# Kernel tuning notes

Measured on AMD Instinct MI355X. Metric: run time of the kernel, lower is better.

## Reference

```python
import jax, jax.numpy as jnp
import numpy as np

B, T, E, H2, V, NT = 256, 192, 300, 256, 11626, 13  # batch, max_len, embed, hidden_dim, vocab, num_tags
START, STOP = 0, 10
NEG = -10000.0


def setup_inputs() -> dict:
    key = jax.random.key(0)
    ks = jax.random.split(key, 13)
    H = H2 // 2
    s = 0.1
    trans = jax.random.normal(ks[12], (NT, NT), dtype=jnp.float32)
    trans = trans.at[START, :].set(NEG).at[:, STOP].set(NEG)
    return {
        "sentence": jax.random.randint(ks[0], (B, T), 0, V),
        "seq_len": jax.random.randint(ks[1], (B,), 1, T + 1),  # lengths >= 1
        "tags": jax.random.randint(ks[2], (B, T), 0, 10),
        "embedding": jax.random.normal(ks[3], (V, E), dtype=jnp.float32) * s,
        "W_ih_f": jax.random.normal(ks[4], (4 * H, E), dtype=jnp.float32) * s,
        "W_hh_f": jax.random.normal(ks[5], (4 * H, H), dtype=jnp.float32) * s,
        "b_f": jnp.zeros((4 * H,), jnp.float32),
        "W_ih_b": jax.random.normal(ks[6], (4 * H, E), dtype=jnp.float32) * s,
        "W_hh_b": jax.random.normal(ks[7], (4 * H, H), dtype=jnp.float32) * s,
        "b_b": jnp.zeros((4 * H,), jnp.float32),
        "W_fc": jax.random.normal(ks[8], (NT, H2), dtype=jnp.float32) * s,
        "b_fc": jnp.zeros((NT,), jnp.float32),
        "transitions": trans,
    }


def _rev_within_len(x, lens):
    # reverse each sequence's first `len` positions (mimics packed-sequence reverse dir)
    t = jnp.arange(x.shape[1])
    idx = jnp.where(t[None, :] < lens[:, None], lens[:, None] - 1 - t[None, :], t[None, :])
    return jnp.take_along_axis(x, idx[:, :, None], axis=1)


def _lstm_dir(x, lens, W_ih, W_hh, b):
    # x: [B,T,E] -> [B,T,H]; PyTorch gate order i,f,g,o; padded steps frozen + zeroed output
    Bx, Tx, _ = x.shape
    H = W_hh.shape[1]
    mask = (jnp.arange(Tx)[None, :] < lens[:, None]).astype(x.dtype)  # [B,T]
    gx = jnp.einsum('bte,ge->btg', x, W_ih) + b  # precompute input projections

    def step(carry, inp):
        h, c = carry
        g_x, m = inp  # [B,4H], [B,1]
        g = g_x + h @ W_hh.T
        i, f, gg, o = jnp.split(g, 4, axis=-1)
        c_new = jax.nn.sigmoid(f) * c + jax.nn.sigmoid(i) * jnp.tanh(gg)
        h_new = jax.nn.sigmoid(o) * jnp.tanh(c_new)
        h = jnp.where(m > 0, h_new, h)
        c = jnp.where(m > 0, c_new, c)
        return (h, c), h * m

    h0 = jnp.zeros((Bx, H), x.dtype)
    _, hs = jax.lax.scan(step, (h0, h0), (gx.transpose(1, 0, 2), mask.T[:, :, None]))
    return hs.transpose(1, 0, 2)


def _crf_nll(feats, tags, transitions):
    # feats: [B,T,NT]; iterate over ALL T padded positions (faithful to source)
    def fwd_step(alpha, feat):
        # alpha_new[b,j] = logsumexp_i(alpha[b,i] + trans[j,i]) + feat[b,j]
        nxt = jax.nn.logsumexp(alpha[:, None, :] + transitions[None, :, :], axis=-1) + feat
        return nxt, None

    alpha0 = jnp.full((feats.shape[0], NT), NEG, feats.dtype).at[:, START].set(0.0)
    alphaT, _ = jax.lax.scan(fwd_step, alpha0, feats.transpose(1, 0, 2))
    fwd_score = jax.nn.logsumexp(alphaT + transitions[STOP][None, :], axis=-1)  # [B]

    tags_ext = jnp.concatenate([jnp.full((feats.shape[0], 1), START, tags.dtype), tags], axis=1)
    trans_sc = transitions[tags_ext[:, 1:], tags_ext[:, :-1]].sum(-1)
    emit_sc = jnp.take_along_axis(feats, tags[:, :, None], axis=2)[:, :, 0].sum(-1)
    gold = trans_sc + emit_sc + transitions[STOP, tags[:, -1]]
    return fwd_score - gold  # [B]


def reference(sentence, seq_len, tags, embedding, W_ih_f, W_hh_f, b_f,
              W_ih_b, W_hh_b, b_b, W_fc, b_fc, transitions):
    lens = jnp.clip(seq_len, 1, T)  # seq_len.clamp(max=192)
    emb = embedding[sentence]  # [B,T,E]
    h_f = _lstm_dir(emb, lens, W_ih_f, W_hh_f, b_f)
    h_b = _rev_within_len(_lstm_dir(_rev_within_len(emb, lens), lens, W_ih_b, W_hh_b, b_b), lens)
    out = jnp.concatenate([h_f, h_b], axis=-1)  # [B,T,H2]
    feats = jnp.einsum('bth,gh->btg', out, W_fc) + b_fc  # [B,T,NT]
    nll = _crf_nll(feats, tags, transitions)
    return nll.mean()
```

## Files before the change

kernel.cpp:

```cpp
#include <hip/hip_runtime.h>
#include <hip/hip_bf16.h>


#define B_   256
#define T_   192
#define E_   300
#define KP   320
#define H_   128
#define G4   512
#define NG   1024
#define NT_  13
#define NEGV -10000.0f
#define HSTR 144

typedef __attribute__((ext_vector_type(8))) short bf16x8;
typedef __attribute__((ext_vector_type(4))) float f32x4;
typedef __attribute__((ext_vector_type(4))) unsigned short u16x4;

__device__ __forceinline__ unsigned short f2bf(float f) {
    return (unsigned short)(__float_as_uint(f) >> 16);
}
__device__ __forceinline__ float bf2f(unsigned short h) {
    return __uint_as_float(((unsigned)h) << 16);
}
__device__ __forceinline__ float sigf(float x) {
    return __builtin_amdgcn_rcpf(1.0f + __expf(-x));
}
__device__ __forceinline__ float tanhfast(float x) {
    return __builtin_amdgcn_rcpf(1.0f + __expf(-2.0f * x)) * 2.0f - 1.0f;
}
__device__ __forceinline__ void barrier_lgkm() {
    asm volatile("s_waitcnt lgkmcnt(0)\n\ts_barrier" ::: "memory");
}

__global__ void pack_kernel(const float* __restrict__ Wf, const float* __restrict__ Wb,
                            const float* __restrict__ Whf, const float* __restrict__ Whb,
                            const float* __restrict__ emb, const int* __restrict__ sent,
                            unsigned short* __restrict__ Wp, unsigned short* __restrict__ Whp,
                            unsigned short* __restrict__ A, float* __restrict__ out) {
    int blk = blockIdx.x;
    int k = threadIdx.x;
    if (blk == 0 && k == 0) out[0] = 0.0f;
    if (blk < NG) {
        float v = 0.0f;
        if (k < E_) v = (blk < G4) ? Wf[blk * E_ + k] : Wb[(blk - G4) * E_ + k];
        Wp[blk * KP + k] = f2bf(v);
    } else if (blk < NG + 1024) {
        int t = blk - NG;
        int d = t >> 9, g = t & 511;
        if (k < H_) {
            const float* src = d ? Whb : Whf;
            float v = src[g * H_ + k];
            int w = (g >> 4) & 7, j = g >> 7, colq = g & 15;
            int kc = k >> 5, quad = (k >> 3) & 3, e = k & 7;
            Whp[((((size_t)(d * 8 + w) * 4 + j) * 4 + kc) * 64 + quad * 16 + colq) * 8 + e] = f2bf(v);
        }
    } else {
        int m = blk - NG - 1024;
        int tok = sent[m];
        float v = 0.0f;
        if (k < E_) v = emb[(size_t)tok * E_ + k];
        A[(size_t)m * KP + k] = f2bf(v);
    }
}

__global__ __launch_bounds__(256, 3) void gemm_kernel(const unsigned short* __restrict__ A,
                                                      const unsigned short* __restrict__ Bw,
                                                      const float* __restrict__ bF,
                                                      const float* __restrict__ bB,
                                                      unsigned short* __restrict__ C) {
    __shared__ __align__(16) unsigned short As[128 * 64];
    __shared__ __align__(16) unsigned short Bs[128 * 64];
    const int tid  = threadIdx.x;
    const int lane = tid & 63;
    const int wave = tid >> 6;
    const int wr = wave >> 1, wc = wave & 1;
    const int colL = lane & 15;
    const int mBase = blockIdx.y * 128;
    const int bx = blockIdx.x;
    const int d  = bx >> 2;
    const int w0 = (bx & 3) * 2;
    f32x4 acc[4][4] = {};
    for (int k0 = 0; k0 < KP; k0 += 64) {
        #pragma unroll
        for (int j = 0; j < 4; j++) {
            int c   = tid + 256 * j;
            int row = c >> 3;
            int col = (c & 7) * 8;
            __builtin_amdgcn_global_load_lds(
                (const void*)(A + (size_t)(mBase + row) * KP + k0 + col),
                (void*)((char*)As + c * 16), 16, 0, 0);
            int ws = row >> 6, jj = (row >> 4) & 3, cc = row & 15;
            int srcrow = d * 512 + (8 * jj + w0 + ws) * 16 + cc;
            __builtin_amdgcn_global_load_lds(
                (const void*)(Bw + (size_t)srcrow * KP + k0 + col),
                (void*)((char*)Bs + c * 16), 16, 0, 0);
        }
        __syncthreads();
        #pragma unroll
        for (int ks = 0; ks < 2; ks++) {
            bf16x8 af[4], bfr[4];
            #pragma unroll
            for (int i = 0; i < 4; i++) {
                int arow = wr * 64 + i * 16 + colL;
                af[i]  = *(const bf16x8*)(As + arow * 64 + ks * 32 + (lane >> 4) * 8);
                int brow = wc * 64 + i * 16 + colL;
                bfr[i] = *(const bf16x8*)(Bs + brow * 64 + ks * 32 + (lane >> 4) * 8);
            }
            #pragma unroll
            for (int i = 0; i < 4; i++)
                #pragma unroll
                for (int n2 = 0; n2 < 4; n2++)
                    acc[i][n2] = __builtin_amdgcn_mfma_f32_16x16x32_bf16(af[i], bfr[n2], acc[i][n2], 0, 0, 0);
        }
        __syncthreads();
    }
    const float* bias_d = d ? bB : bF;
    float bj[4];
    #pragma unroll
    for (int n2 = 0; n2 < 4; n2++) bj[n2] = bias_d[(8 * n2 + w0 + wc) * 16 + colL];
    #pragma unroll
    for (int i = 0; i < 4; i++)
        #pragma unroll
        for (int r = 0; r < 4; r++) {
            int row = mBase + wr * 64 + i * 16 + (lane >> 4) * 4 + r;
            u16x4 v;
            #pragma unroll
            for (int n2 = 0; n2 < 4; n2++) v[n2] = f2bf(acc[i][n2][r] + bj[n2]);
            *(u16x4*)(C + (size_t)row * NG + d * 512 + (w0 + wc) * 64 + colL * 4) = v;
        }
}

__global__ __launch_bounds__(576, 1) void lstm_kernel(const unsigned short* __restrict__ gxP,
                                                      const unsigned short* __restrict__ Whp,
                                                      const int* __restrict__ seq_len,
                                                      const float* __restrict__ Wfc,
                                                      float* __restrict__ featsF,
                                                      float* __restrict__ featsB) {
    __shared__ __align__(16) unsigned short hL[2][16 * HSTR];
    __shared__ int Ls[4];
    __shared__ int maxLs;
    const int tid  = threadIdx.x;
    const int wave = tid >> 6;
    const int lane = tid & 63;
    const int col  = lane & 15;
    const int quad = lane >> 4;
    const int dir  = blockIdx.x & 1;
    const int b0   = (blockIdx.x >> 1) * 4;
    float* fOut = dir ? featsB : featsF;

    if (tid < 4) Ls[tid] = min(max(seq_len[b0 + tid], 1), T_);
    __syncthreads();
    if (tid == 0) { int m = 0; for (int i = 0; i < 4; i++) m = max(m, Ls[i]); maxLs = m; }
    __syncthreads();
    const int maxL = maxLs;
    const int Lq = Ls[quad];
    const int dNG = dir ? -NG : NG;

    bf16x8 Bf[4][4];
    bf16x8 Wf8[4];
    const unsigned short* rb = nullptr;
    int ofs2 = 0;
    u16x4 gx0v = {}, gx1v = {};
    float* fb = nullptr;
    int foff = 0;

    if (wave < 8) {
        #pragma unroll
        for (int j = 0; j < 4; j++)
            #pragma unroll
            for (int kc = 0; kc < 4; kc++)
                Bf[j][kc] = *(const bf16x8*)(Whp +
                    ((((size_t)(dir * 8 + wave) * 4 + j) * 4 + kc) * 64 + lane) * 8);
        int row = b0 + quad;
        int p0 = dir ? (Lq - 1) : 0;
        rb = gxP + ((size_t)(row * T_ + p0)) * NG + dir * 512 + wave * 64 + col * 4;
        gx0v = *(const u16x4*)(rb);
        gx1v = *(const u16x4*)(rb + ((Lq > 1) ? dNG : 0));
        ofs2 = min(2, Lq - 1) * dNG;
    } else {
        #pragma unroll
        for (int kc = 0; kc < 4; kc++)
            #pragma unroll
            for (int e = 0; e < 8; e++) {
                float v = (col < NT_) ? Wfc[col * 256 + dir * H_ + kc * 32 + quad * 8 + e] : 0.0f;
                Wf8[kc][e] = (short)f2bf(v);
            }
        fb = fOut + (size_t)(b0 + quad) * T_ * NT_ + col;
        foff = (dir ? (Lq - 1) : 0) * NT_;
    }
    const int fd = dir ? -NT_ : NT_;

    float cst = 0.0f;
    bf16x8 Af[4];
    #pragma unroll
    for (int kc = 0; kc < 4; kc++)
        #pragma unroll
        for (int e = 0; e < 8; e++) Af[kc][e] = 0;

    auto step_body = [&](int s, u16x4& gxs, int par) {
        if (wave < 8) {
            f32x4 acc[4];
            #pragma unroll
            for (int j = 0; j < 4; j++) {
                acc[j][0] = bf2f(gxs[j]);
                acc[j][1] = 0.f; acc[j][2] = 0.f; acc[j][3] = 0.f;
            }
            gxs = *(const u16x4*)(rb + ofs2);
            ofs2 = (s + 3 < Lq) ? ofs2 + dNG : ofs2;
            #pragma unroll
            for (int kc = 0; kc < 4; kc++)
                #pragma unroll
                for (int j = 0; j < 4; j++)
                    acc[j] = __builtin_amdgcn_mfma_f32_16x16x32_bf16(Af[kc], Bf[j][kc], acc[j], 0, 0, 0);
            float cn = sigf(acc[1][0]) * cst + sigf(acc[0][0]) * tanhfast(acc[2][0]);
            cst = cn;
            float hn = sigf(acc[3][0]) * tanhfast(cn);
            hL[par][(quad * 4) * HSTR + wave * 16 + col] = f2bf(hn);
        }
        barrier_lgkm();
        #pragma unroll
        for (int kc = 0; kc < 4; kc++)
            Af[kc] = *(const bf16x8*)(&hL[par][col * HSTR + kc * 32 + quad * 8]);
        if (wave == 8) {
            f32x4 fc = (f32x4){0.f, 0.f, 0.f, 0.f};
            #pragma unroll
            for (int kc = 0; kc < 4; kc++)
                fc = __builtin_amdgcn_mfma_f32_16x16x32_bf16(Af[kc], Wf8[kc], fc, 0, 0, 0);
            if (col < NT_ && s < Lq) fb[foff] = fc[0];
            foff += fd;
        }
    };

    for (int s = 0; s < maxL; s += 2) {
        step_body(s, gx0v, 0);
        if (s + 1 < maxL) step_body(s + 1, gx1v, 1);
    }
}

__global__ __launch_bounds__(64) void crf_kernel(const float* __restrict__ fF,
                                                 const float* __restrict__ fB,
                                                 const float* __restrict__ bfc,
                                                 const float* __restrict__ trans,
                                                 const int* __restrict__ tags,
                                                 const int* __restrict__ seq_len,
                                                 float* __restrict__ out) {
    __shared__ __align__(16) float feat_lds[2 * 208];
    __shared__ float Tlds[NT_ * NT_];
    const int lane = threadIdx.x;
    const int b = blockIdx.x;
    const int Lb = min(max(seq_len[b], 1), T_);
    const float* fFb = fF + (size_t)b * T_ * NT_;
    const float* fBb = fB + (size_t)b * T_ * NT_;
    const int* tg = tags + (size_t)b * T_;

    for (int i = lane; i < NT_ * NT_; i += 64) Tlds[i] = trans[i];

    const int jc = min(lane, NT_ - 1);
    float Tj[NT_];
    #pragma unroll
    for (int i = 0; i < NT_; i++) Tj[i] = trans[jc * NT_ + i];
    const float bj  = bfc[jc];
    const float T10 = trans[10 * NT_ + jc];
    float alj = (jc == 0 && lane == 0) ? 0.0f : NEGV;

    const int e0 = lane * 4;
    const bool ldact = (lane < 52);
    float4 vF = {}, vB = {};
    if (ldact) { vF = *(const float4*)(fFb + e0); vB = *(const float4*)(fBb + e0); }

    #pragma unroll 1
    for (int c = 0; c < 12; ++c) {
        if (ldact) {
            float4 w;
            #pragma unroll
            for (int k = 0; k < 4; k++) {
                unsigned g = (unsigned)(c * 208 + e0 + k);
                unsigned t = g / 13u;
                float s = ((const float*)&vF)[k] + ((const float*)&vB)[k];
                ((float*)&w)[k] = (t < (unsigned)Lb) ? s : 0.0f;
            }
            *(float4*)&feat_lds[(c & 1) * 208 + e0] = w;
            if (c < 11) {
                vF = *(const float4*)(fFb + (c + 1) * 208 + e0);
                vB = *(const float4*)(fBb + (c + 1) * 208 + e0);
            }
        }
        barrier_lgkm();
        const int fbase = (c & 1) * 208;
        for (int tt = 0; tt < 16; ++tt) {
            float a0  = __shfl(alj, 0, 64),  a1  = __shfl(alj, 1, 64);
            float a2  = __shfl(alj, 2, 64),  a3  = __shfl(alj, 3, 64);
            float a4  = __shfl(alj, 4, 64),  a5  = __shfl(alj, 5, 64);
            float a6  = __shfl(alj, 6, 64),  a7  = __shfl(alj, 7, 64);
            float a8  = __shfl(alj, 8, 64),  a9  = __shfl(alj, 9, 64);
            float a10 = __shfl(alj, 10, 64), a11 = __shfl(alj, 11, 64);
            float a12 = __shfl(alj, 12, 64);
            float feat = feat_lds[fbase + tt * NT_ + jc];
            float v0 = a0 + Tj[0],  v1 = a1 + Tj[1],  v2 = a2 + Tj[2],  v3 = a3 + Tj[3];
            float v4 = a4 + Tj[4],  v5 = a5 + Tj[5],  v6 = a6 + Tj[6],  v7 = a7 + Tj[7];
            float v8 = a8 + Tj[8],  v9 = a9 + Tj[9],  v10 = a10 + Tj[10], v11 = a11 + Tj[11];
            float v12 = a12 + Tj[12];
            float p0 = fmaxf(v0, v1), p1 = fmaxf(v2, v3), p2 = fmaxf(v4, v5);
            float p3 = fmaxf(v6, v7), p4 = fmaxf(v8, v9), p5 = fmaxf(v10, v11);
            float q0 = fmaxf(p0, p1), q1 = fmaxf(p2, p3), q2 = fmaxf(p4, p5);
            float m = fmaxf(fmaxf(q0, q1), fmaxf(q2, v12));
            float e0_ = __expf(v0 - m),  e1_ = __expf(v1 - m),  e2_ = __expf(v2 - m);
            float e3_ = __expf(v3 - m),  e4_ = __expf(v4 - m),  e5_ = __expf(v5 - m);
            float e6_ = __expf(v6 - m),  e7_ = __expf(v7 - m),  e8_ = __expf(v8 - m);
            float e9_ = __expf(v9 - m),  e10_ = __expf(v10 - m), e11_ = __expf(v11 - m);
            float e12_ = __expf(v12 - m);
            float s0 = e0_ + e1_, s1 = e2_ + e3_, s2 = e4_ + e5_, s3 = e6_ + e7_;
            float s4 = e8_ + e9_, s5 = e10_ + e11_;
            float u0 = s0 + s1, u1 = s2 + s3, u2 = s4 + s5;
            float ss = (u0 + u1) + (u2 + e12_);
            alj = m + __logf(ss) + feat + bj;
        }
    }

    float gp = 0.0f;
    #pragma unroll
    for (int u = 0; u < 3; ++u) {
        int t = lane + u * 64;
        int tt_ = tg[t];
        int pv = (t == 0) ? 0 : tg[t - 1];
        float e = bfc[tt_];
        if (t < Lb) e += fFb[t * NT_ + tt_] + fBb[t * NT_ + tt_];
        gp += Tlds[tt_ * NT_ + pv] + e;
    }
    #pragma unroll
    for (int o = 32; o > 0; o >>= 1) gp += __shfl_down(gp, o, 64);

    float vj = (lane < NT_) ? (alj + T10) : -3.0e38f;
    float mm = vj;
    #pragma unroll
    for (int o = 32; o > 0; o >>= 1) mm = fmaxf(mm, __shfl_down(mm, o, 64));
    mm = __shfl(mm, 0, 64);
    float se = (lane < NT_) ? __expf(vj - mm) : 0.0f;
    #pragma unroll
    for (int o = 32; o > 0; o >>= 1) se += __shfl_down(se, o, 64);
    if (lane == 0) {
        float fwd = mm + __logf(se);
        float gold = gp + Tlds[10 * NT_ + tg[T_ - 1]];
        atomicAdd(out, (fwd - gold) * (1.0f / 256.0f));
    }
}

extern "C" void kernel_launch(void* const* d_in, const int* in_sizes, int n_in,
                              void* d_out, int out_size, void* d_ws, size_t ws_size,
                              hipStream_t stream) {
    const int*   sentence  = (const int*)d_in[0];
    const int*   seq_len   = (const int*)d_in[1];
    const int*   tags      = (const int*)d_in[2];
    const float* embedding = (const float*)d_in[3];
    const float* W_ih_f    = (const float*)d_in[4];
    const float* W_hh_f    = (const float*)d_in[5];
    const float* b_f       = (const float*)d_in[6];
    const float* W_ih_b    = (const float*)d_in[7];
    const float* W_hh_b    = (const float*)d_in[8];
    const float* b_b       = (const float*)d_in[9];
    const float* W_fc      = (const float*)d_in[10];
    const float* b_fc      = (const float*)d_in[11];
    const float* trans     = (const float*)d_in[12];
    float* out = (float*)d_out;

    char* ws = (char*)d_ws;
    const size_t M = (size_t)B_ * T_;
    unsigned short* Wp    = (unsigned short*)(ws);
    unsigned short* Ap    = (unsigned short*)(ws + 655360);
    unsigned short* gx    = (unsigned short*)(ws + 32112640);
    float* featsF = (float*)(ws + 132775936);
    float* featsB = (float*)(ws + 135331840);
    unsigned short* Whp   = (unsigned short*)(ws + 137887744);

    pack_kernel<<<NG + 1024 + (int)M, KP, 0, stream>>>(W_ih_f, W_ih_b, W_hh_f, W_hh_b,
                                                       embedding, sentence, Wp, Whp, Ap, out);
    dim3 gg(8, (int)(M / 128));
    gemm_kernel<<<gg, 256, 0, stream>>>(Ap, Wp, b_f, b_b, gx);
    lstm_kernel<<<128, 576, 0, stream>>>(gx, Whp, seq_len, W_fc, featsF, featsB);
    crf_kernel<<<B_, 64, 0, stream>>>(featsF, featsB, b_fc, trans, tags, seq_len, out);
}
```

Baseline: 329.6 us.

## Gather embeddings inside GEMM from packed vocab table; process two batches per CRF block

The pack kernel now converts the whole embedding table (V rows) to bf16 instead of materialising a gathered B*T activation matrix. The GEMM gathers rows by token id directly into LDS, which removes a large write and read of the intermediate. The CRF kernel handles two sequences per wavefront, interleaving their independent recurrences to hide shuffle and transcendental latency, at the cost of half as many blocks.

```diff
diff --git a/kernel.cpp b/kernel.cpp
--- a/kernel.cpp
+++ b/kernel.cpp
@@ -6,6 +6,7 @@
 #define T_   192
 #define E_   300
 #define KP   320
+#define V_   11626
 #define H_   128
 #define G4   512
 #define NG   1024
@@ -35,9 +36,9 @@
 
 __global__ void pack_kernel(const float* __restrict__ Wf, const float* __restrict__ Wb,
                             const float* __restrict__ Whf, const float* __restrict__ Whb,
-                            const float* __restrict__ emb, const int* __restrict__ sent,
+                            const float* __restrict__ emb,
                             unsigned short* __restrict__ Wp, unsigned short* __restrict__ Whp,
-                            unsigned short* __restrict__ A, float* __restrict__ out) {
+                            unsigned short* __restrict__ Ep, float* __restrict__ out) {
     int blk = blockIdx.x;
     int k = threadIdx.x;
     if (blk == 0 && k == 0) out[0] = 0.0f;
@@ -56,15 +57,14 @@
             Whp[((((size_t)(d * 8 + w) * 4 + j) * 4 + kc) * 64 + quad * 16 + colq) * 8 + e] = f2bf(v);
         }
     } else {
-        int m = blk - NG - 1024;
-        int tok = sent[m];
-        float v = 0.0f;
-        if (k < E_) v = emb[(size_t)tok * E_ + k];
-        A[(size_t)m * KP + k] = f2bf(v);
-    }
-}
-
-__global__ __launch_bounds__(256, 3) void gemm_kernel(const unsigned short* __restrict__ A,
+        int r = blk - NG - 1024;
+        float v = (k < E_) ? emb[(size_t)r * E_ + k] : 0.0f;
+        Ep[(size_t)r * KP + k] = f2bf(v);
+    }
+}
+
+__global__ __launch_bounds__(256, 3) void gemm_kernel(const unsigned short* __restrict__ Ep,
+                                                      const int* __restrict__ sent,
                                                       const unsigned short* __restrict__ Bw,
                                                       const float* __restrict__ bF,
                                                       const float* __restrict__ bB,
@@ -80,6 +80,10 @@
     const int bx = blockIdx.x;
     const int d  = bx >> 2;
     const int w0 = (bx & 3) * 2;
+    int toks[4];
+    #pragma unroll
+    for (int j = 0; j < 4; j++)
+        toks[j] = sent[mBase + ((tid + 256 * j) >> 3)];
     f32x4 acc[4][4] = {};
     for (int k0 = 0; k0 < KP; k0 += 64) {
         #pragma unroll
@@ -88,7 +92,7 @@
             int row = c >> 3;
             int col = (c & 7) * 8;
             __builtin_amdgcn_global_load_lds(
-                (const void*)(A + (size_t)(mBase + row) * KP + k0 + col),
+                (const void*)(Ep + (size_t)toks[j] * KP + k0 + col),
                 (void*)((char*)As + c * 16), 16, 0, 0);
             int ws = row >> 6, jj = (row >> 4) & 3, cc = row & 15;
             int srcrow = d * 512 + (8 * jj + w0 + ws) * 16 + cc;
@@ -245,14 +249,18 @@
                                                  const int* __restrict__ tags,
                                                  const int* __restrict__ seq_len,
                                                  float* __restrict__ out) {
-    __shared__ __align__(16) float feat_lds[2 * 208];
+    __shared__ __align__(16) float feat_lds[2][2][208];
     __shared__ float Tlds[NT_ * NT_];
     const int lane = threadIdx.x;
-    const int b = blockIdx.x;
-    const int Lb = min(max(seq_len[b], 1), T_);
-    const float* fFb = fF + (size_t)b * T_ * NT_;
-    const float* fBb = fB + (size_t)b * T_ * NT_;
-    const int* tg = tags + (size_t)b * T_;
+    const int bA = blockIdx.x * 2, bB = bA + 1;
+    const int LbA = min(max(seq_len[bA], 1), T_);
+    const int LbB = min(max(seq_len[bB], 1), T_);
+    const float* fF0 = fF + (size_t)bA * T_ * NT_;
+    const float* fB0 = fB + (size_t)bA * T_ * NT_;
+    const float* fF1 = fF + (size_t)bB * T_ * NT_;
+    const float* fB1 = fB + (size_t)bB * T_ * NT_;
+    const int* tgA = tags + (size_t)bA * T_;
+    const int* tgB = tags + (size_t)bB * T_;
 
     for (int i = lane; i < NT_ * NT_; i += 64) Tlds[i] = trans[i];
 
@@ -262,87 +270,111 @@
     for (int i = 0; i < NT_; i++) Tj[i] = trans[jc * NT_ + i];
     const float bj  = bfc[jc];
     const float T10 = trans[10 * NT_ + jc];
-    float alj = (jc == 0 && lane == 0) ? 0.0f : NEGV;
+    float alA = (lane == 0) ? 0.0f : NEGV;
+    float alB = (lane == 0) ? 0.0f : NEGV;
 
     const int e0 = lane * 4;
     const bool ldact = (lane < 52);
-    float4 vF = {}, vB = {};
-    if (ldact) { vF = *(const float4*)(fFb + e0); vB = *(const float4*)(fBb + e0); }
+    float4 vF0 = {}, vB0 = {}, vF1 = {}, vB1 = {};
+    if (ldact) {
+        vF0 = *(const float4*)(fF0 + e0); vB0 = *(const float4*)(fB0 + e0);
+        vF1 = *(const float4*)(fF1 + e0); vB1 = *(const float4*)(fB1 + e0);
+    }
 
     #pragma unroll 1
     for (int c = 0; c < 12; ++c) {
         if (ldact) {
-            float4 w;
+            float4 w0, w1;
             #pragma unroll
             for (int k = 0; k < 4; k++) {
                 unsigned g = (unsigned)(c * 208 + e0 + k);
                 unsigned t = g / 13u;
-                float s = ((const float*)&vF)[k] + ((const float*)&vB)[k];
-                ((float*)&w)[k] = (t < (unsigned)Lb) ? s : 0.0f;
-            }
-            *(float4*)&feat_lds[(c & 1) * 208 + e0] = w;
+                float s0 = ((const float*)&vF0)[k] + ((const float*)&vB0)[k];
+                float s1 = ((const float*)&vF1)[k] + ((const float*)&vB1)[k];
+                ((float*)&w0)[k] = (t < (unsigned)LbA) ? s0 : 0.0f;
+                ((float*)&w1)[k] = (t < (unsigned)LbB) ? s1 : 0.0f;
+            }
+            *(float4*)&feat_lds[c & 1][0][e0] = w0;
+            *(float4*)&feat_lds[c & 1][1][e0] = w1;
             if (c < 11) {
-                vF = *(const float4*)(fFb + (c + 1) * 208 + e0);
-                vB = *(const float4*)(fBb + (c + 1) * 208 + e0);
+                vF0 = *(const float4*)(fF0 + (c + 1) * 208 + e0);
+                vB0 = *(const float4*)(fB0 + (c + 1) * 208 + e0);
+                vF1 = *(const float4*)(fF1 + (c + 1) * 208 + e0);
+                vB1 = *(const float4*)(fB1 + (c + 1) * 208 + e0);
             }
         }
         barrier_lgkm();
-        const int fbase = (c & 1) * 208;
+        const int par = c & 1;
         for (int tt = 0; tt < 16; ++tt) {
-            float a0  = __shfl(alj, 0, 64),  a1  = __shfl(alj, 1, 64);
-            float a2  = __shfl(alj, 2, 64),  a3  = __shfl(alj, 3, 64);
-            float a4  = __shfl(alj, 4, 64),  a5  = __shfl(alj, 5, 64);
-            float a6  = __shfl(alj, 6, 64),  a7  = __shfl(alj, 7, 64);
-            float a8  = __shfl(alj, 8, 64),  a9  = __shfl(alj, 9, 64);
-            float a10 = __shfl(alj, 10, 64), a11 = __shfl(alj, 11, 64);
-            float a12 = __shfl(alj, 12, 64);
-            float feat = feat_lds[fbase + tt * NT_ + jc];
-            float v0 = a0 + Tj[0],  v1 = a1 + Tj[1],  v2 = a2 + Tj[2],  v3 = a3 + Tj[3];
-            float v4 = a4 + Tj[4],  v5 = a5 + Tj[5],  v6 = a6 + Tj[6],  v7 = a7 + Tj[7];
-            float v8 = a8 + Tj[8],  v9 = a9 + Tj[9],  v10 = a10 + Tj[10], v11 = a11 + Tj[11];
-            float v12 = a12 + Tj[12];
-            float p0 = fmaxf(v0, v1), p1 = fmaxf(v2, v3), p2 = fmaxf(v4, v5);
-            float p3 = fmaxf(v6, v7), p4 = fmaxf(v8, v9), p5 = fmaxf(v10, v11);
-            float q0 = fmaxf(p0, p1), q1 = fmaxf(p2, p3), q2 = fmaxf(p4, p5);
-            float m = fmaxf(fmaxf(q0, q1), fmaxf(q2, v12));
-            float e0_ = __expf(v0 - m),  e1_ = __expf(v1 - m),  e2_ = __expf(v2 - m);
-            float e3_ = __expf(v3 - m),  e4_ = __expf(v4 - m),  e5_ = __expf(v5 - m);
-            float e6_ = __expf(v6 - m),  e7_ = __expf(v7 - m),  e8_ = __expf(v8 - m);
-            float e9_ = __expf(v9 - m),  e10_ = __expf(v10 - m), e11_ = __expf(v11 - m);
-            float e12_ = __expf(v12 - m);
-            float s0 = e0_ + e1_, s1 = e2_ + e3_, s2 = e4_ + e5_, s3 = e6_ + e7_;
-            float s4 = e8_ + e9_, s5 = e10_ + e11_;
-            float u0 = s0 + s1, u1 = s2 + s3, u2 = s4 + s5;
-            float ss = (u0 + u1) + (u2 + e12_);
-            alj = m + __logf(ss) + feat + bj;
-        }
-    }
-
-    float gp = 0.0f;
+            float featA = feat_lds[par][0][tt * NT_ + jc];
+            float featB = feat_lds[par][1][tt * NT_ + jc];
+            float vA[NT_], vB_[NT_];
+            #pragma unroll
+            for (int i = 0; i < NT_; i++) {
+                vA[i]  = __shfl(alA, i, 64) + Tj[i];
+                vB_[i] = __shfl(alB, i, 64) + Tj[i];
+            }
+            float mA = vA[12], mB = vB_[12];
+            #pragma unroll
+            for (int i = 0; i < 12; i += 2) {
+                mA = fmaxf(mA, fmaxf(vA[i], vA[i + 1]));
+                mB = fmaxf(mB, fmaxf(vB_[i], vB_[i + 1]));
+            }
+            float sA = 0.0f, sB = 0.0f;
+            #pragma unroll
+            for (int i = 0; i < NT_; i++) {
+                sA += __expf(vA[i] - mA);
+                sB += __expf(vB_[i] - mB);
+            }
+            alA = mA + __logf(sA) + featA + bj;
+            alB = mB + __logf(sB) + featB + bj;
+        }
+    }
+
+    float gpA = 0.0f, gpB = 0.0f;
     #pragma unroll
     for (int u = 0; u < 3; ++u) {
         int t = lane + u * 64;
-        int tt_ = tg[t];
-        int pv = (t == 0) ? 0 : tg[t - 1];
-        float e = bfc[tt_];
-        if (t < Lb) e += fFb[t * NT_ + tt_] + fBb[t * NT_ + tt_];
-        gp += Tlds[tt_ * NT_ + pv] + e;
-    }
-    #pragma unroll
-    for (int o = 32; o > 0; o >>= 1) gp += __shfl_down(gp, o, 64);
-
-    float vj = (lane < NT_) ? (alj + T10) : -3.0e38f;
-    float mm = vj;
-    #pragma unroll
-    for (int o = 32; o > 0; o >>= 1) mm = fmaxf(mm, __shfl_down(mm, o, 64));
-    mm = __shfl(mm, 0, 64);
-    float se = (lane < NT_) ? __expf(vj - mm) : 0.0f;
-    #pragma unroll
-    for (int o = 32; o > 0; o >>= 1) se += __shfl_down(se, o, 64);
+        int ta = tgA[t];
+        int pa = (t == 0) ? 0 : tgA[t - 1];
+        float ea = bfc[ta];
+        if (t < LbA) ea += fF0[t * NT_ + ta] + fB0[t * NT_ + ta];
+        gpA += Tlds[ta * NT_ + pa] + ea;
+        int tb = tgB[t];
+        int pb = (t == 0) ? 0 : tgB[t - 1];
+        float eb = bfc[tb];
+        if (t < LbB) eb += fF1[t * NT_ + tb] + fB1[t * NT_ + tb];
+        gpB += Tlds[tb * NT_ + pb] + eb;
+    }
+    #pragma unroll
+    for (int o = 32; o > 0; o >>= 1) {
+        gpA += __shfl_down(gpA, o, 64);
+        gpB += __shfl_down(gpB, o, 64);
+    }
+
+    float vjA = (lane < NT_) ? (alA + T10) : -3.0e38f;
+    float vjB = (lane < NT_) ? (alB + T10) : -3.0e38f;
+    float mmA = vjA, mmB = vjB;
+    #pragma unroll
+    for (int o = 32; o > 0; o >>= 1) {
+        mmA = fmaxf(mmA, __shfl_down(mmA, o, 64));
+        mmB = fmaxf(mmB, __shfl_down(mmB, o, 64));
+    }
+    mmA = __shfl(mmA, 0, 64);
+    mmB = __shfl(mmB, 0, 64);
+    float seA = (lane < NT_) ? __expf(vjA - mmA) : 0.0f;
+    float seB = (lane < NT_) ? __expf(vjB - mmB) : 0.0f;
+    #pragma unroll
+    for (int o = 32; o > 0; o >>= 1) {
+        seA += __shfl_down(seA, o, 64);
+        seB += __shfl_down(seB, o, 64);
+    }
     if (lane == 0) {
-        float fwd = mm + __logf(se);
-        float gold = gp + Tlds[10 * NT_ + tg[T_ - 1]];
-        atomicAdd(out, (fwd - gold) * (1.0f / 256.0f));
+        float fwdA = mmA + __logf(seA);
+        float fwdB = mmB + __logf(seB);
+        float goldA = gpA + Tlds[10 * NT_ + tgA[T_ - 1]];
+        float goldB = gpB + Tlds[10 * NT_ + tgB[T_ - 1]];
+        atomicAdd(out, ((fwdA - goldA) + (fwdB - goldB)) * (1.0f / 256.0f));
     }
 }
 
@@ -366,17 +398,17 @@
 
     char* ws = (char*)d_ws;
     const size_t M = (size_t)B_ * T_;
-    unsigned short* Wp    = (unsigned short*)(ws);
-    unsigned short* Ap    = (unsigned short*)(ws + 655360);
-    unsigned short* gx    = (unsigned short*)(ws + 32112640);
-    float* featsF = (float*)(ws + 132775936);
-    float* featsB = (float*)(ws + 135331840);
-    unsigned short* Whp   = (unsigned short*)(ws + 137887744);
-
-    pack_kernel<<<NG + 1024 + (int)M, KP, 0, stream>>>(W_ih_f, W_ih_b, W_hh_f, W_hh_b,
-                                                       embedding, sentence, Wp, Whp, Ap, out);
+    unsigned short* Wp  = (unsigned short*)(ws);
+    unsigned short* Ep  = (unsigned short*)(ws + 655360);
+    unsigned short* gx  = (unsigned short*)(ws + 8096000);
+    float* featsF = (float*)(ws + 108759296);
+    float* featsB = (float*)(ws + 111315200);
+    unsigned short* Whp = (unsigned short*)(ws + 113871104);
+
+    pack_kernel<<<NG + 1024 + V_, KP, 0, stream>>>(W_ih_f, W_ih_b, W_hh_f, W_hh_b,
+                                                   embedding, Wp, Whp, Ep, out);
     dim3 gg(8, (int)(M / 128));
-    gemm_kernel<<<gg, 256, 0, stream>>>(Ap, Wp, b_f, b_b, gx);
+    gemm_kernel<<<gg, 256, 0, stream>>>(Ep, sentence, Wp, b_f, b_b, gx);
     lstm_kernel<<<128, 576, 0, stream>>>(gx, Whp, seq_len, W_fc, featsF, featsB);
-    crf_kernel<<<B_, 64, 0, stream>>>(featsF, featsB, b_fc, trans, tags, seq_len, out);
-}
+    crf_kernel<<<B_ / 2, 64, 0, stream>>>(featsF, featsB, b_fc, trans, tags, seq_len, out);
+}
```

Measured after the change: 343.8 us. +4.3%, slower.
